# Kernel tuning notes

Measured on AMD Instinct MI355X. Metric: run time of the kernel, lower is better.

## Reference

```python
import jax, jax.numpy as jnp
import numpy as np

BLOCK_SPLIT = (4, 4, 4)
GRID = 256
N_BLOCK = 64
BX = GRID // 4  # 64, per-block grid resolution along each axis
N_PTS = 4_194_304


def setup_inputs() -> dict:
    key = jax.random.key(0)
    k1, k2 = jax.random.split(key)
    aabb = jnp.array([[-1.5, -1.5, -1.5], [1.5, 1.5, 1.5]], dtype=jnp.float32)
    # points roughly inside the aabb
    xyz_sampled = jax.random.uniform(k1, (N_PTS, 3), dtype=jnp.float32) * 3.0 - 1.5
    alpha_volume = jax.random.uniform(k2, (GRID, GRID, GRID), dtype=jnp.float32)
    # per-block domains (as kilonerf global_to_local expects): block AABBs
    idx = np.stack(np.meshgrid(np.arange(4), np.arange(4), np.arange(4), indexing='ij'), -1).reshape(-1, 3)
    voxel = np.array([3.0 / 4.0] * 3)
    dmin = (-1.5 + idx * voxel).astype(np.float32)
    dmax = (dmin + voxel).astype(np.float32)
    return {"xyz_sampled": xyz_sampled, "aabb": aabb, "alpha_volume": alpha_volume,
            "domain_min": jnp.asarray(dmin), "domain_max": jnp.asarray(dmax)}


def _sample_alpha(xyz, aabb, alpha_volume, dmin, dmax):
    bs = jnp.asarray(BLOCK_SPLIT, jnp.float32)
    voxel = (aabb[1] - aabb[0]) / bs                      # per-block world size
    idx3 = jnp.floor((xyz - aabb[0]) / voxel).astype(jnp.int32)
    idx3 = jnp.clip(idx3, 0, jnp.array(BLOCK_SPLIT, jnp.int32) - 1)  # edge clamp (matches loop)
    strides = jnp.array([BLOCK_SPLIT[2] * BLOCK_SPLIT[1], BLOCK_SPLIT[2], 1], jnp.int32)
    bid = (idx3 * strides).sum(-1)                        # [N] block id in [0, 64)

    order = jnp.argsort(bid)                              # jax sort is stable; matches bucket-by-block order
    bid_s = bid[order]
    pts = xyz[order]

    # global_to_local (kilonerf): map into per-block [-1,1]^3
    local = 2.0 * (pts - dmin[bid_s]) / (dmax[bid_s] - dmin[bid_s]) - 1.0  # [N,3] (gx,gy,gz)

    # torch .view(64,1,64,64,64) is a raw contiguous reinterpretation -> plain reshape
    vols = alpha_volume.reshape(N_BLOCK, BX, BX, BX)      # [B, D, H, W]
    D = H = W = BX
    # grid_sample convention: grid x -> W axis, y -> H axis, z -> D axis; align_corners=True
    fx = (local[:, 0] + 1.0) * 0.5 * (W - 1)
    fy = (local[:, 1] + 1.0) * 0.5 * (H - 1)
    fz = (local[:, 2] + 1.0) * 0.5 * (D - 1)
    x0 = jnp.floor(fx); y0 = jnp.floor(fy); z0 = jnp.floor(fz)
    wx = fx - x0; wy = fy - y0; wz = fz - z0
    x0i = x0.astype(jnp.int32); y0i = y0.astype(jnp.int32); z0i = z0.astype(jnp.int32)

    def fetch(zi, yi, xi):
        # zeros padding for out-of-range corners (grid_sample padding_mode='zeros')
        inb = (zi >= 0) & (zi < D) & (yi >= 0) & (yi < H) & (xi >= 0) & (xi < W)
        v = vols[bid_s, jnp.clip(zi, 0, D - 1), jnp.clip(yi, 0, H - 1), jnp.clip(xi, 0, W - 1)]
        return jnp.where(inb, v, 0.0)

    out = jnp.zeros_like(fx)
    for dz, wz_ in ((0, 1.0 - wz), (1, wz)):
        for dy, wy_ in ((0, 1.0 - wy), (1, wy)):
            for dx, wx_ in ((0, 1.0 - wx), (1, wx)):
                out = out + wz_ * wy_ * wx_ * fetch(z0i + dz, y0i + dy, x0i + dx)
    return out  # [N] alpha values in block-sorted order


def reference(xyz_sampled, aabb, alpha_volume, domain_min, domain_max):
    return _sample_alpha(xyz_sampled, aabb, alpha_volume, domain_min, domain_max)
```

## Files before the change

### kernel.cpp

```cpp
#include <hip/hip_runtime.h>

#define TILE  4096
#define BLK   256
#define NBUCK 64

__device__ __forceinline__ int compute_bid(float px, float py, float pz,
                                           float a0x, float a0y, float a0z,
                                           float vx, float vy, float vz) {
    int ix = (int)floorf((px - a0x) / vx);
    int iy = (int)floorf((py - a0y) / vy);
    int iz = (int)floorf((pz - a0z) / vz);
    ix = min(max(ix, 0), 3);
    iy = min(max(iy, 0), 3);
    iz = min(max(iz, 0), 3);
    return ix * 16 + iy * 4 + iz;
}

__global__ void hist_kernel(const float* __restrict__ xyz,
                            const float* __restrict__ aabb,
                            int* __restrict__ hist, int N, int G) {
    __shared__ int s_h[NBUCK];
    const int tid = threadIdx.x, g = blockIdx.x;
    if (tid < NBUCK) s_h[tid] = 0;
    __syncthreads();
    const float a0x = aabb[0], a0y = aabb[1], a0z = aabb[2];
    const float vx = (aabb[3] - a0x) * 0.25f;
    const float vy = (aabb[4] - a0y) * 0.25f;
    const float vz = (aabb[5] - a0z) * 0.25f;
    for (int c = 0; c < TILE / BLK; ++c) {
        int i = g * TILE + c * BLK + tid;
        if (i < N) {
            float px = xyz[3 * i], py = xyz[3 * i + 1], pz = xyz[3 * i + 2];
            int b = compute_bid(px, py, pz, a0x, a0y, a0z, vx, vy, vz);
            atomicAdd(&s_h[b], 1);
        }
    }
    __syncthreads();
    if (tid < NBUCK) hist[tid * G + g] = s_h[tid];
}

__global__ void scan_rows_kernel(int* __restrict__ hist, int* __restrict__ tot, int G) {
    __shared__ int sh[BLK];
    const int b = blockIdx.x, t = threadIdx.x;
    const int L = (G + BLK - 1) / BLK;
    const int lo = t * L;
    const int n = min(L, max(0, G - lo));
    const int base = b * G + lo;
    int s = 0;
    for (int k = 0; k < n; ++k) s += hist[base + k];
    sh[t] = s;
    __syncthreads();
    for (int off = 1; off < BLK; off <<= 1) {
        int v = (t >= off) ? sh[t - off] : 0;
        __syncthreads();
        sh[t] += v;
        __syncthreads();
    }
    int excl = (t == 0) ? 0 : sh[t - 1];
    for (int k = 0; k < n; ++k) {
        int v = hist[base + k];
        hist[base + k] = excl;
        excl += v;
    }
    if (t == BLK - 1) tot[b] = sh[BLK - 1];
}

__global__ void scan_buckets_kernel(const int* __restrict__ tot, int* __restrict__ off) {
    __shared__ int sh[NBUCK];
    const int t = threadIdx.x;
    sh[t] = tot[t];
    __syncthreads();
    for (int o = 1; o < NBUCK; o <<= 1) {
        int v = (t >= o) ? sh[t - o] : 0;
        __syncthreads();
        sh[t] += v;
        __syncthreads();
    }
    off[t] = (t == 0) ? 0 : sh[t - 1];
}

__global__ void scatter_perm_kernel(const float* __restrict__ xyz,
                                    const float* __restrict__ aabb,
                                    const int* __restrict__ hist,
                                    const int* __restrict__ off,
                                    int* __restrict__ perm, int N, int G) {
    __shared__ int s_cnt[NBUCK];
    __shared__ int s_whist[4][NBUCK];
    const int tid = threadIdx.x, g = blockIdx.x;
    if (tid < NBUCK) s_cnt[tid] = hist[tid * G + g] + off[tid];
    const float a0x = aabb[0], a0y = aabb[1], a0z = aabb[2];
    const float vx = (aabb[3] - a0x) * 0.25f;
    const float vy = (aabb[4] - a0y) * 0.25f;
    const float vz = (aabb[5] - a0z) * 0.25f;
    __syncthreads();

    const int lane = tid & 63;
    const int wv = tid >> 6;
    const unsigned long long lt = (1ull << lane) - 1ull;

    for (int c = 0; c < TILE / BLK; ++c) {
        int i = g * TILE + c * BLK + tid;
        bool valid = (i < N);
        int b = 0;
        if (valid) {
            float px = xyz[3 * i], py = xyz[3 * i + 1], pz = xyz[3 * i + 2];
            b = compute_bid(px, py, pz, a0x, a0y, a0z, vx, vy, vz);
        }
        ((int*)s_whist)[tid] = 0;
        __syncthreads();
        unsigned long long m = __ballot(valid);
        #pragma unroll
        for (int k = 0; k < 6; ++k) {
            unsigned long long bal = __ballot((b >> k) & 1);
            m &= ((b >> k) & 1) ? bal : ~bal;
        }
        int rank = __popcll(m & lt);
        if (valid && rank == 0) s_whist[wv][b] = __popcll(m);
        __syncthreads();
        if (valid) {
            int pos = s_cnt[b] + rank;
            for (int w2 = 0; w2 < wv; ++w2) pos += s_whist[w2][b];
            perm[pos] = i;
        }
        __syncthreads();
        if (tid < NBUCK)
            s_cnt[tid] += s_whist[0][tid] + s_whist[1][tid] +
                          s_whist[2][tid] + s_whist[3][tid];
        __syncthreads();
    }
}

__global__ void gather_out_kernel(const float* __restrict__ xyz,
                                  const float* __restrict__ aabb,
                                  const float* __restrict__ vol,
                                  const float* __restrict__ dmin,
                                  const float* __restrict__ dmax,
                                  const int* __restrict__ perm,
                                  float* __restrict__ out, int N) {
    __shared__ float s_dmin[192], s_dmax[192];
    const int tid = threadIdx.x;
    for (int i = tid; i < 192; i += BLK) {
        s_dmin[i] = dmin[i];
        s_dmax[i] = dmax[i];
    }
    int nb = gridDim.x;
    int d = blockIdx.x;
    int lb = (nb % 8 == 0) ? (d % 8) * (nb / 8) + (d / 8) : d;
    const float a0x = aabb[0], a0y = aabb[1], a0z = aabb[2];
    const float vx = (aabb[3] - a0x) * 0.25f;
    const float vy = (aabb[4] - a0y) * 0.25f;
    const float vz = (aabb[5] - a0z) * 0.25f;
    __syncthreads();

    int j = lb * BLK + tid;
    if (j >= N) return;
    int i = perm[j];
    float px = xyz[3 * i], py = xyz[3 * i + 1], pz = xyz[3 * i + 2];
    int b = compute_bid(px, py, pz, a0x, a0y, a0z, vx, vy, vz);
    float dn0 = s_dmin[3 * b], dn1 = s_dmin[3 * b + 1], dn2 = s_dmin[3 * b + 2];
    float dM0 = s_dmax[3 * b], dM1 = s_dmax[3 * b + 1], dM2 = s_dmax[3 * b + 2];
    float lx = 2.0f * (px - dn0) / (dM0 - dn0) - 1.0f;
    float ly = 2.0f * (py - dn1) / (dM1 - dn1) - 1.0f;
    float lz = 2.0f * (pz - dn2) / (dM2 - dn2) - 1.0f;
    float fx = (lx + 1.0f) * 0.5f * 63.0f;
    float fy = (ly + 1.0f) * 0.5f * 63.0f;
    float fz = (lz + 1.0f) * 0.5f * 63.0f;
    float x0f = floorf(fx), y0f = floorf(fy), z0f = floorf(fz);
    float wx = fx - x0f, wy = fy - y0f, wz = fz - z0f;
    int x0 = (int)x0f, y0 = (int)y0f, z0 = (int)z0f;
    const float* vb = vol + ((size_t)b << 18);
    auto F = [&](int zi, int yi, int xi) -> float {
        if ((unsigned)zi >= 64u || (unsigned)yi >= 64u || (unsigned)xi >= 64u)
            return 0.0f;
        return vb[(zi << 12) + (yi << 6) + xi];
    };
    float s = 0.0f;
    s += (1.0f - wz) * (1.0f - wy) * (1.0f - wx) * F(z0,     y0,     x0);
    s += (1.0f - wz) * (1.0f - wy) * wx          * F(z0,     y0,     x0 + 1);
    s += (1.0f - wz) * wy          * (1.0f - wx) * F(z0,     y0 + 1, x0);
    s += (1.0f - wz) * wy          * wx          * F(z0,     y0 + 1, x0 + 1);
    s += wz          * (1.0f - wy) * (1.0f - wx) * F(z0 + 1, y0,     x0);
    s += wz          * (1.0f - wy) * wx          * F(z0 + 1, y0,     x0 + 1);
    s += wz          * wy          * (1.0f - wx) * F(z0 + 1, y0 + 1, x0);
    s += wz          * wy          * wx          * F(z0 + 1, y0 + 1, x0 + 1);
    out[j] = s;
}

extern "C" void kernel_launch(void* const* d_in, const int* in_sizes, int n_in,
                              void* d_out, int out_size, void* d_ws, size_t ws_size,
                              hipStream_t stream) {
    const float* xyz  = (const float*)d_in[0];
    const float* aabb = (const float*)d_in[1];
    const float* vol  = (const float*)d_in[2];
    const float* dmin = (const float*)d_in[3];
    const float* dmax = (const float*)d_in[4];
    float* out = (float*)d_out;
    const int N = in_sizes[0] / 3;
    const int G = (N + TILE - 1) / TILE;

    char* ws = (char*)d_ws;
    int* hist = (int*)ws;
    int* tot  = (int*)(ws + (size_t)NBUCK * G * 4);
    int* off  = (int*)(ws + (size_t)NBUCK * G * 4 + 256);
    int* perm = (int*)(ws + (size_t)NBUCK * G * 4 + 512);

    hist_kernel<<<G, BLK, 0, stream>>>(xyz, aabb, hist, N, G);
    scan_rows_kernel<<<NBUCK, BLK, 0, stream>>>(hist, tot, G);
    scan_buckets_kernel<<<1, NBUCK, 0, stream>>>(tot, off);
    scatter_perm_kernel<<<G, BLK, 0, stream>>>(xyz, aabb, hist, off, perm, N, G);
    gather_out_kernel<<<(N + BLK - 1) / BLK, BLK, 0, stream>>>(
        xyz, aabb, vol, dmin, dmax, perm, out, N);
}
```

Before: 308.5 us.

## Scatter precomputed sample coords as float4 payload instead of permutation indices

The scatter pass now computes the per-block grid coordinates and block id and writes them as a 16-byte payload at the sorted position. The gather kernel then reads that payload contiguously instead of following a permutation index into xyz with random reads. The histogram kernel also loads four points at a time through float4 vector reads. The cost is a 16-byte scattered write per point instead of a 4-byte one, and a larger workspace.

```diff
diff --git a/kernel.cpp b/kernel.cpp
--- a/kernel.cpp
+++ b/kernel.cpp
@@ -27,12 +27,28 @@
     const float vx = (aabb[3] - a0x) * 0.25f;
     const float vy = (aabb[4] - a0y) * 0.25f;
     const float vz = (aabb[5] - a0z) * 0.25f;
-    for (int c = 0; c < TILE / BLK; ++c) {
-        int i = g * TILE + c * BLK + tid;
-        if (i < N) {
-            float px = xyz[3 * i], py = xyz[3 * i + 1], pz = xyz[3 * i + 2];
-            int b = compute_bid(px, py, pz, a0x, a0y, a0z, vx, vy, vz);
-            atomicAdd(&s_h[b], 1);
+    for (int c = 0; c < TILE / (BLK * 4); ++c) {
+        int p0 = g * TILE + c * (BLK * 4) + tid * 4;
+        if (p0 + 3 < N) {
+            const float4* v4 = (const float4*)(xyz + (size_t)p0 * 3);
+            float4 f0 = v4[0], f1 = v4[1], f2 = v4[2];
+            int b0 = compute_bid(f0.x, f0.y, f0.z, a0x, a0y, a0z, vx, vy, vz);
+            int b1 = compute_bid(f0.w, f1.x, f1.y, a0x, a0y, a0z, vx, vy, vz);
+            int b2 = compute_bid(f1.z, f1.w, f2.x, a0x, a0y, a0z, vx, vy, vz);
+            int b3 = compute_bid(f2.y, f2.z, f2.w, a0x, a0y, a0z, vx, vy, vz);
+            atomicAdd(&s_h[b0], 1);
+            atomicAdd(&s_h[b1], 1);
+            atomicAdd(&s_h[b2], 1);
+            atomicAdd(&s_h[b3], 1);
+        } else {
+            for (int k = 0; k < 4; ++k) {
+                int i = p0 + k;
+                if (i < N) {
+                    int b = compute_bid(xyz[3 * i], xyz[3 * i + 1], xyz[3 * i + 2],
+                                        a0x, a0y, a0z, vx, vy, vz);
+                    atomicAdd(&s_h[b], 1);
+                }
+            }
         }
     }
     __syncthreads();
@@ -79,15 +95,22 @@
     off[t] = (t == 0) ? 0 : sh[t - 1];
 }
 
-__global__ void scatter_perm_kernel(const float* __restrict__ xyz,
-                                    const float* __restrict__ aabb,
-                                    const int* __restrict__ hist,
-                                    const int* __restrict__ off,
-                                    int* __restrict__ perm, int N, int G) {
-    __shared__ int s_cnt[NBUCK];
-    __shared__ int s_whist[4][NBUCK];
+__global__ void scatter_payload_kernel(const float* __restrict__ xyz,
+                                       const float* __restrict__ aabb,
+                                       const float* __restrict__ dmin,
+                                       const float* __restrict__ dmax,
+                                       const int* __restrict__ hist,
+                                       const int* __restrict__ off,
+                                       float4* __restrict__ payload, int N, int G) {
+    __shared__ int   s_cnt[NBUCK];
+    __shared__ int   s_whist[4][NBUCK];
+    __shared__ float s_dmin[192], s_dmax[192];
     const int tid = threadIdx.x, g = blockIdx.x;
     if (tid < NBUCK) s_cnt[tid] = hist[tid * G + g] + off[tid];
+    for (int i = tid; i < 192; i += BLK) {
+        s_dmin[i] = dmin[i];
+        s_dmax[i] = dmax[i];
+    }
     const float a0x = aabb[0], a0y = aabb[1], a0z = aabb[2];
     const float vx = (aabb[3] - a0x) * 0.25f;
     const float vy = (aabb[4] - a0y) * 0.25f;
@@ -102,9 +125,18 @@
         int i = g * TILE + c * BLK + tid;
         bool valid = (i < N);
         int b = 0;
+        float fx = 0.0f, fy = 0.0f, fz = 0.0f;
         if (valid) {
             float px = xyz[3 * i], py = xyz[3 * i + 1], pz = xyz[3 * i + 2];
             b = compute_bid(px, py, pz, a0x, a0y, a0z, vx, vy, vz);
+            float dn0 = s_dmin[3 * b], dn1 = s_dmin[3 * b + 1], dn2 = s_dmin[3 * b + 2];
+            float dM0 = s_dmax[3 * b], dM1 = s_dmax[3 * b + 1], dM2 = s_dmax[3 * b + 2];
+            float lx = 2.0f * (px - dn0) / (dM0 - dn0) - 1.0f;
+            float ly = 2.0f * (py - dn1) / (dM1 - dn1) - 1.0f;
+            float lz = 2.0f * (pz - dn2) / (dM2 - dn2) - 1.0f;
+            fx = (lx + 1.0f) * 0.5f * 63.0f;
+            fy = (ly + 1.0f) * 0.5f * 63.0f;
+            fz = (lz + 1.0f) * 0.5f * 63.0f;
         }
         ((int*)s_whist)[tid] = 0;
         __syncthreads();
@@ -120,7 +152,7 @@
         if (valid) {
             int pos = s_cnt[b] + rank;
             for (int w2 = 0; w2 < wv; ++w2) pos += s_whist[w2][b];
-            perm[pos] = i;
+            payload[pos] = make_float4(fx, fy, fz, __int_as_float(b));
         }
         __syncthreads();
         if (tid < NBUCK)
@@ -130,41 +162,17 @@
     }
 }
 
-__global__ void gather_out_kernel(const float* __restrict__ xyz,
-                                  const float* __restrict__ aabb,
-                                  const float* __restrict__ vol,
-                                  const float* __restrict__ dmin,
-                                  const float* __restrict__ dmax,
-                                  const int* __restrict__ perm,
+__global__ void gather_out_kernel(const float* __restrict__ vol,
+                                  const float4* __restrict__ payload,
                                   float* __restrict__ out, int N) {
-    __shared__ float s_dmin[192], s_dmax[192];
-    const int tid = threadIdx.x;
-    for (int i = tid; i < 192; i += BLK) {
-        s_dmin[i] = dmin[i];
-        s_dmax[i] = dmax[i];
-    }
     int nb = gridDim.x;
     int d = blockIdx.x;
     int lb = (nb % 8 == 0) ? (d % 8) * (nb / 8) + (d / 8) : d;
-    const float a0x = aabb[0], a0y = aabb[1], a0z = aabb[2];
-    const float vx = (aabb[3] - a0x) * 0.25f;
-    const float vy = (aabb[4] - a0y) * 0.25f;
-    const float vz = (aabb[5] - a0z) * 0.25f;
-    __syncthreads();
-
-    int j = lb * BLK + tid;
+    int j = lb * BLK + threadIdx.x;
     if (j >= N) return;
-    int i = perm[j];
-    float px = xyz[3 * i], py = xyz[3 * i + 1], pz = xyz[3 * i + 2];
-    int b = compute_bid(px, py, pz, a0x, a0y, a0z, vx, vy, vz);
-    float dn0 = s_dmin[3 * b], dn1 = s_dmin[3 * b + 1], dn2 = s_dmin[3 * b + 2];
-    float dM0 = s_dmax[3 * b], dM1 = s_dmax[3 * b + 1], dM2 = s_dmax[3 * b + 2];
-    float lx = 2.0f * (px - dn0) / (dM0 - dn0) - 1.0f;
-    float ly = 2.0f * (py - dn1) / (dM1 - dn1) - 1.0f;
-    float lz = 2.0f * (pz - dn2) / (dM2 - dn2) - 1.0f;
-    float fx = (lx + 1.0f) * 0.5f * 63.0f;
-    float fy = (ly + 1.0f) * 0.5f * 63.0f;
-    float fz = (lz + 1.0f) * 0.5f * 63.0f;
+    float4 p = payload[j];
+    float fx = p.x, fy = p.y, fz = p.z;
+    int b = __float_as_int(p.w);
     float x0f = floorf(fx), y0f = floorf(fy), z0f = floorf(fz);
     float wx = fx - x0f, wy = fy - y0f, wz = fz - z0f;
     int x0 = (int)x0f, y0 = (int)y0f, z0 = (int)z0f;
@@ -199,15 +207,15 @@
     const int G = (N + TILE - 1) / TILE;
 
     char* ws = (char*)d_ws;
-    int* hist = (int*)ws;
-    int* tot  = (int*)(ws + (size_t)NBUCK * G * 4);
-    int* off  = (int*)(ws + (size_t)NBUCK * G * 4 + 256);
-    int* perm = (int*)(ws + (size_t)NBUCK * G * 4 + 512);
+    float4* payload = (float4*)ws;
+    int* hist = (int*)(ws + (size_t)N * 16);
+    int* tot  = (int*)(ws + (size_t)N * 16 + (size_t)NBUCK * G * 4);
+    int* off  = (int*)(ws + (size_t)N * 16 + (size_t)NBUCK * G * 4 + 256);
 
     hist_kernel<<<G, BLK, 0, stream>>>(xyz, aabb, hist, N, G);
     scan_rows_kernel<<<NBUCK, BLK, 0, stream>>>(hist, tot, G);
     scan_buckets_kernel<<<1, NBUCK, 0, stream>>>(tot, off);
-    scatter_perm_kernel<<<G, BLK, 0, stream>>>(xyz, aabb, hist, off, perm, N, G);
-    gather_out_kernel<<<(N + BLK - 1) / BLK, BLK, 0, stream>>>(
-        xyz, aabb, vol, dmin, dmax, perm, out, N);
-}
+    scatter_payload_kernel<<<G, BLK, 0, stream>>>(xyz, aabb, dmin, dmax, hist, off,
+                                                  payload, N, G);
+    gather_out_kernel<<<(N + BLK - 1) / BLK, BLK, 0, stream>>>(vol, payload, out, N);
+}
```

Result: faster. 292.0 us (-5.3%).
